# Kernel optimization log

Measured on AMD Instinct MI355X. Metric: run time of the kernel, lower is better.

The kernel has to match this reference:

```python
import jax, jax.numpy as jnp
import numpy as np

HIDDEN = 1024
SINK = 4
RECENT = 19  # int(window_size=64 * 0.3)
COMPRESSION_RATIO = 0.5


def setup_inputs() -> dict:
    key = jax.random.key(0)
    ks = jax.random.split(key, 10)
    B, S, H = 4, 4096, HIDDEN
    xav = lambda k, fi, fo: jax.random.normal(k, (fi, fo), jnp.float32) * np.sqrt(2.0 / (fi + fo))
    return {
        'keys': jax.random.normal(ks[0], (B, S, H), jnp.float32),
        'values': jax.random.normal(ks[1], (B, S, H), jnp.float32),
        # attention_predictor: Linear(H, H//2) -> ReLU -> Linear(H//2, 1) -> Sigmoid
        'W1a': xav(ks[2], H, H // 2), 'b1a': jnp.zeros((H // 2,), jnp.float32),
        'W2a': xav(ks[3], H // 2, 1), 'b2a': jnp.zeros((1,), jnp.float32),
        # importance_estimator: Linear(H, H//4) -> ReLU -> Linear(H//4, 1)
        'W1i': xav(ks[4], H, H // 4), 'b1i': jnp.zeros((H // 4,), jnp.float32),
        'W2i': xav(ks[5], H // 4, 1), 'b2i': jnp.zeros((1,), jnp.float32),
    }


def _token_scores(keys, values, W1a, b1a, W2a, b2a, W1i, b1i, W2i, b2i):
    att = jax.nn.sigmoid(jnp.einsum('bsh,ho->bso', jax.nn.relu(keys @ W1a + b1a), W2a) + b2a)[..., 0]
    imp = (jnp.einsum('bsh,ho->bso', jax.nn.relu(values @ W1i + b1i), W2i) + b2i)[..., 0]
    return 0.6 * att + 0.4 * imp  # [B, S]


def _selection_mask(scores):
    B, S = scores.shape
    keep_count = max(int(S * (1.0 - COMPRESSION_RATIO)), SINK + RECENT)
    mask = jnp.zeros((B, S), dtype=bool)
    mask = mask.at[:, :SINK].set(True)
    mask = mask.at[:, S - RECENT:].set(True)
    mid_len = S - RECENT - SINK
    if mid_len > 0:
        middle_keep = keep_count - SINK - RECENT
        if middle_keep > 0:
            k = min(middle_keep, mid_len)
            _, idx = jax.lax.top_k(scores[:, SINK:S - RECENT], k)  # [B, k]
            rows = jnp.arange(B)[:, None]
            mask = mask.at[rows, idx + SINK].set(True)
    return mask


def reference(keys, values, W1a, b1a, W2a, b2a, W1i, b1i, W2i, b2i):
    scores = _token_scores(keys, values, W1a, b1a, W2a, b2a, W1i, b1i, W2i, b2i)
    mask = _selection_mask(scores).astype(keys.dtype)[..., None]  # [B, S, 1]
    return keys * mask, values * mask
```

## Files before the change

kernel.cpp:

```cpp
#include <hip/hip_runtime.h>
#include <math.h>

#define H      1024
#define NA     512
#define NI     256
#define SEQ    4096
#define BATCH  4
#define NTOK   (BATCH*SEQ)
#define MTOK   16
#define KC     8
#define PT     20
#define SINKN  4
#define RECENTN 19
#define MIDN   (SEQ - SINKN - RECENTN)
#define KSEL   2025
#define CHK    16

__global__ __launch_bounds__(256, 4) void score_kernel(
    const float* __restrict__ keys, const float* __restrict__ values,
    const float* __restrict__ W1a, const float* __restrict__ b1a,
    const float* __restrict__ W2a, const float* __restrict__ b2a,
    const float* __restrict__ W1i, const float* __restrict__ b1i,
    const float* __restrict__ W2i, const float* __restrict__ b2i,
    float* __restrict__ scores)
{
    __shared__ __align__(16) float smem[KC * NA + KC * NI + 2 * KC * PT];
    float* wa_lds = smem;
    float* wi_lds = smem + KC * NA;
    float* k_lds  = smem + KC * (NA + NI);
    float* v_lds  = k_lds + KC * PT;

    const int tid  = threadIdx.x;
    const int to   = tid & 63;
    const int tt   = tid >> 6;
    const int tokb = blockIdx.x * MTOK;

    float accA0[4][4], accA1[4][4], accI[4][4];
#pragma unroll
    for (int j = 0; j < 4; ++j)
#pragma unroll
        for (int t = 0; t < 4; ++t) { accA0[j][t] = 0.f; accA1[j][t] = 0.f; accI[j][t] = 0.f; }

    const bool st_on = (tid & 3) == 0;
    const int  item  = tid >> 2;
    const int  st_t  = item & 15;
    const int  st_q  = (item >> 4) & 1;
    const bool st_v  = (item >> 5) & 1;
    const float* st_src = (st_v ? values : keys) + (size_t)(tokb + st_t) * H + st_q * 4;
    float* st_dst = (st_v ? v_lds : k_lds);

    for (int h0 = 0; h0 < H; h0 += KC) {
        const float4* wap = (const float4*)(W1a + (size_t)h0 * NA);
        const float4* wip = (const float4*)(W1i + (size_t)h0 * NI);
        float4 wb0 = wap[tid];
        float4 wb1 = wap[tid + 256];
        float4 wb2 = wap[tid + 512];
        float4 wb3 = wap[tid + 768];
        float4 ib0 = wip[tid];
        float4 ib1 = wip[tid + 256];
        float4 tk;
        if (st_on) tk = *(const float4*)(st_src + h0);

        __syncthreads();
        ((float4*)wa_lds)[tid      ] = wb0;
        ((float4*)wa_lds)[tid + 256] = wb1;
        ((float4*)wa_lds)[tid + 512] = wb2;
        ((float4*)wa_lds)[tid + 768] = wb3;
        ((float4*)wi_lds)[tid      ] = ib0;
        ((float4*)wi_lds)[tid + 256] = ib1;
        if (st_on) {
            st_dst[(st_q * 4 + 0) * PT + st_t] = tk.x;
            st_dst[(st_q * 4 + 1) * PT + st_t] = tk.y;
            st_dst[(st_q * 4 + 2) * PT + st_t] = tk.z;
            st_dst[(st_q * 4 + 3) * PT + st_t] = tk.w;
        }
        __syncthreads();

#pragma unroll
        for (int h = 0; h < KC; ++h) {
            float kf[4], vf[4], wa[8], wi4[4];
            *(float4*)&kf[0]  = *(const float4*)&k_lds[h * PT + tt * 4];
            *(float4*)&vf[0]  = *(const float4*)&v_lds[h * PT + tt * 4];
            *(float4*)&wa[0]  = *(const float4*)&wa_lds[h * NA + to * 4];
            *(float4*)&wa[4]  = *(const float4*)&wa_lds[h * NA + 256 + to * 4];
            *(float4*)&wi4[0] = *(const float4*)&wi_lds[h * NI + to * 4];
#pragma unroll
            for (int j = 0; j < 4; ++j)
#pragma unroll
                for (int t = 0; t < 4; ++t) {
                    accA0[j][t] = fmaf(kf[t], wa[j],     accA0[j][t]);
                    accA1[j][t] = fmaf(kf[t], wa[4 + j], accA1[j][t]);
                    accI[j][t]  = fmaf(vf[t], wi4[j],    accI[j][t]);
                }
        }
    }

    float b1aA[8], w2aA[8], b1iA[4], w2iA[4];
    *(float4*)&b1aA[0] = *(const float4*)(b1a + to * 4);
    *(float4*)&b1aA[4] = *(const float4*)(b1a + 256 + to * 4);
    *(float4*)&w2aA[0] = *(const float4*)(W2a + to * 4);
    *(float4*)&w2aA[4] = *(const float4*)(W2a + 256 + to * 4);
    *(float4*)&b1iA[0] = *(const float4*)(b1i + to * 4);
    *(float4*)&w2iA[0] = *(const float4*)(W2i + to * 4);

    __syncthreads();
    float* red_a = smem;
    float* red_i = smem + 16 * 65;

#pragma unroll
    for (int t = 0; t < 4; ++t) {
        float pa = 0.f, pi = 0.f;
#pragma unroll
        for (int j = 0; j < 4; ++j) {
            pa += fmaxf(accA0[j][t] + b1aA[j],     0.f) * w2aA[j];
            pa += fmaxf(accA1[j][t] + b1aA[4 + j], 0.f) * w2aA[4 + j];
            pi += fmaxf(accI[j][t]  + b1iA[j],     0.f) * w2iA[j];
        }
        const int tg = tt * 4 + t;
        red_a[tg * 65 + to] = pa;
        red_i[tg * 65 + to] = pi;
    }
    __syncthreads();
    if (tid < MTOK) {
        float sa = 0.f, si = 0.f;
        for (int j2 = 0; j2 < 64; ++j2) {
            sa += red_a[tid * 65 + j2];
            si += red_i[tid * 65 + j2];
        }
        const float att = 1.f / (1.f + expf(-(sa + b2a[0])));
        scores[tokb + tid] = 0.6f * att + 0.4f * (si + b2i[0]);
    }
}

__device__ __forceinline__ int block_sum(int val, int* red, int tid)
{
#pragma unroll
    for (int off = 32; off > 0; off >>= 1) val += __shfl_down(val, off);
    if ((tid & 63) == 0) red[tid >> 6] = val;
    __syncthreads();
    const int total = red[0] + red[1] + red[2] + red[3];
    __syncthreads();
    return total;
}

__global__ __launch_bounds__(256) void select_kernel(
    const float* __restrict__ scores, float* __restrict__ mask)
{
    __shared__ unsigned int ks[MIDN];
    __shared__ int hist[256];
    __shared__ int red[4];
    __shared__ int scan_s[256];
    __shared__ unsigned int sh_pref;
    __shared__ int sh_r;

    const int tid = threadIdx.x;
    const int row = blockIdx.x;
    const float* sr = scores + row * SEQ;

    for (int i = tid; i < MIDN; i += 256) {
        unsigned int u = __float_as_uint(sr[SINKN + i]);
        u = (u & 0x80000000u) ? ~u : (u | 0x80000000u);
        ks[i] = u;
    }
    if (tid == 0) { sh_pref = 0u; sh_r = KSEL; }
    __syncthreads();

    for (int b = 3; b >= 0; --b) {
        hist[tid] = 0;
        __syncthreads();
        const unsigned int hi_mask = (b == 3) ? 0u : (0xFFFFFFFFu << ((b + 1) * 8));
        const unsigned int pref = sh_pref;
        for (int i = tid; i < MIDN; i += 256) {
            const unsigned int u = ks[i];
            if ((u & hi_mask) == pref)
                atomicAdd(&hist[(u >> (b * 8)) & 255], 1);
        }
        __syncthreads();

        scan_s[tid] = hist[tid];
        __syncthreads();
#pragma unroll
        for (int off = 1; off < 256; off <<= 1) {
            const int add = (tid + off < 256) ? scan_s[tid + off] : 0;
            __syncthreads();
            scan_s[tid] += add;
            __syncthreads();
        }
        const int r    = sh_r;
        const int sfx  = scan_s[tid];
        const int sfx1 = (tid < 255) ? scan_s[tid + 1] : 0;
        if (sfx >= r && sfx1 < r) {
            sh_r = r - sfx1;
            sh_pref = pref | ((unsigned int)tid << (b * 8));
        }
        __syncthreads();
    }
    const unsigned int v = sh_pref;

    const int st = tid * CHK;
    const int en = (st + CHK < MIDN) ? (st + CHK) : MIDN;

    int cgt = 0, ceq = 0;
    for (int k = st; k < en; ++k) { cgt += (ks[k] > v) ? 1 : 0; ceq += (ks[k] == v) ? 1 : 0; }
    const int total_gt = block_sum(cgt, red, tid);
    const int need = KSEL - total_gt;

    scan_s[tid] = ceq;
    __syncthreads();
#pragma unroll
    for (int off = 1; off < 256; off <<= 1) {
        const int add = (tid >= off) ? scan_s[tid - off] : 0;
        __syncthreads();
        scan_s[tid] += add;
        __syncthreads();
    }
    int r = scan_s[tid] - ceq;

    float* mr = mask + row * SEQ;
    for (int k = st; k < en; ++k) {
        const unsigned int u = ks[k];
        bool keep = false;
        if (u > v) keep = true;
        else if (u == v) { keep = (r < need); ++r; }
        mr[SINKN + k] = keep ? 1.f : 0.f;
    }
    for (int s = tid; s < SEQ; s += 256) {
        if (s < SINKN || s >= SEQ - RECENTN) mr[s] = 1.f;
    }
}

__global__ __launch_bounds__(256) void apply_kernel(
    const float* __restrict__ keys, const float* __restrict__ values,
    const float* __restrict__ mask, float* __restrict__ out)
{
    const int QT = NTOK * H / 4;
    const int stride = gridDim.x * 256;
    for (int i4 = blockIdx.x * 256 + threadIdx.x; i4 < 2 * QT; i4 += stride) {
        const bool isv = (i4 >= QT);
        const int  j4  = isv ? (i4 - QT) : i4;
        const float m  = mask[j4 >> 8];
        const float4* src = isv ? (const float4*)values : (const float4*)keys;
        const float4 x = src[j4];
        float4 y; y.x = x.x * m; y.y = x.y * m; y.z = x.z * m; y.w = x.w * m;
        ((float4*)out)[i4] = y;
    }
}

extern "C" void kernel_launch(void* const* d_in, const int* in_sizes, int n_in,
                              void* d_out, int out_size, void* d_ws, size_t ws_size,
                              hipStream_t stream)
{
    const float* keys   = (const float*)d_in[0];
    const float* values = (const float*)d_in[1];
    const float* W1a = (const float*)d_in[2];
    const float* b1a = (const float*)d_in[3];
    const float* W2a = (const float*)d_in[4];
    const float* b2a = (const float*)d_in[5];
    const float* W1i = (const float*)d_in[6];
    const float* b1i = (const float*)d_in[7];
    const float* W2i = (const float*)d_in[8];
    const float* b2i = (const float*)d_in[9];

    float* scores = (float*)d_ws;
    float* mask   = scores + NTOK;

    score_kernel<<<NTOK / MTOK, 256, 0, stream>>>(keys, values, W1a, b1a, W2a, b2a,
                                                  W1i, b1i, W2i, b2i, scores);
    select_kernel<<<BATCH, 256, 0, stream>>>(scores, mask);
    apply_kernel<<<8192, 256, 0, stream>>>(keys, values, mask, (float*)d_out);
}
```

Baseline: 635.6 us.

## Retile score MLP as 128x128 register-blocked GEMM with per-slice partial outputs

```diff
diff --git a/kernel.cpp b/kernel.cpp
--- a/kernel.cpp
+++ b/kernel.cpp
@@ -7,128 +7,126 @@
 #define SEQ    4096
 #define BATCH  4
 #define NTOK   (BATCH*SEQ)
-#define MTOK   16
-#define KC     8
-#define PT     20
 #define SINKN  4
 #define RECENTN 19
 #define MIDN   (SEQ - SINKN - RECENTN)
 #define KSEL   2025
 #define CHK    16
 
-__global__ __launch_bounds__(256, 4) void score_kernel(
+#define TT   128
+#define UT   128
+#define KC   32
+#define PTA  132
+#define ATT_BLOCKS ((NTOK/TT) * (NA/UT))
+#define IMP_BLOCKS ((NTOK/TT) * (NI/UT))
+
+__global__ __launch_bounds__(256, 3) void score_gemm_kernel(
     const float* __restrict__ keys, const float* __restrict__ values,
     const float* __restrict__ W1a, const float* __restrict__ b1a,
-    const float* __restrict__ W2a, const float* __restrict__ b2a,
+    const float* __restrict__ W2a,
     const float* __restrict__ W1i, const float* __restrict__ b1i,
-    const float* __restrict__ W2i, const float* __restrict__ b2i,
-    float* __restrict__ scores)
-{
-    __shared__ __align__(16) float smem[KC * NA + KC * NI + 2 * KC * PT];
-    float* wa_lds = smem;
-    float* wi_lds = smem + KC * NA;
-    float* k_lds  = smem + KC * (NA + NI);
-    float* v_lds  = k_lds + KC * PT;
-
-    const int tid  = threadIdx.x;
-    const int to   = tid & 63;
-    const int tt   = tid >> 6;
-    const int tokb = blockIdx.x * MTOK;
-
-    float accA0[4][4], accA1[4][4], accI[4][4];
-#pragma unroll
-    for (int j = 0; j < 4; ++j)
-#pragma unroll
-        for (int t = 0; t < 4; ++t) { accA0[j][t] = 0.f; accA1[j][t] = 0.f; accI[j][t] = 0.f; }
-
-    const bool st_on = (tid & 3) == 0;
-    const int  item  = tid >> 2;
-    const int  st_t  = item & 15;
-    const int  st_q  = (item >> 4) & 1;
-    const bool st_v  = (item >> 5) & 1;
-    const float* st_src = (st_v ? values : keys) + (size_t)(tokb + st_t) * H + st_q * 4;
-    float* st_dst = (st_v ? v_lds : k_lds);
+    const float* __restrict__ W2i,
+    float* __restrict__ part)
+{
+    __shared__ __align__(16) float smem[KC * PTA + KC * UT];
+    float* A_lds = smem;
+    float* B_lds = smem + KC * PTA;
+
+    const int tid = threadIdx.x;
+    const int tx  = tid & 15;
+    const int ty  = tid >> 4;
+    const int bid = blockIdx.x;
+
+    const bool is_att = bid < ATT_BLOCKS;
+    const int  lb     = is_att ? bid : bid - ATT_BLOCKS;
+    const int  tile   = is_att ? (lb >> 2) : (lb >> 1);
+    const int  pass   = is_att ? (lb & 3)  : (lb & 1);
+    const int  slot   = is_att ? pass : 4 + pass;
+    const int  tokb   = tile * TT;
+    const int  u0     = pass * UT;
+    const int  wstride = is_att ? NA : NI;
+
+    const float* Aptr = is_att ? keys : values;
+    const float* Wptr = (is_att ? W1a : W1i) + u0;
+    const float* b1p  = (is_att ? b1a : b1i) + u0;
+    const float* w2p  = (is_att ? W2a : W2i) + u0;
+
+    float acc[8][8];
+#pragma unroll
+    for (int t = 0; t < 8; ++t)
+#pragma unroll
+        for (int u = 0; u < 8; ++u) acc[t][u] = 0.f;
+
+    const int at = tid >> 3;
+    const int aq = tid & 7;
+    const float* a_base = Aptr + (size_t)(tokb + at) * H + aq * 4;
+    const int bu = (tid & 31) * 4;
+    const int rb = tid >> 5;
+    const float* b_base = Wptr + (size_t)rb * wstride + bu;
+    const int bq   = bu >> 2;
+    const int bpos = ((bq ^ (bq >> 3)) << 2);
+    const int q1 = 2 * tx, q2 = 2 * tx + 1;
+    const int boff1 = ((q1 ^ (q1 >> 3)) << 2);
+    const int boff2 = ((q2 ^ (q2 >> 3)) << 2);
 
     for (int h0 = 0; h0 < H; h0 += KC) {
-        const float4* wap = (const float4*)(W1a + (size_t)h0 * NA);
-        const float4* wip = (const float4*)(W1i + (size_t)h0 * NI);
-        float4 wb0 = wap[tid];
-        float4 wb1 = wap[tid + 256];
-        float4 wb2 = wap[tid + 512];
-        float4 wb3 = wap[tid + 768];
-        float4 ib0 = wip[tid];
-        float4 ib1 = wip[tid + 256];
-        float4 tk;
-        if (st_on) tk = *(const float4*)(st_src + h0);
-
-        __syncthreads();
-        ((float4*)wa_lds)[tid      ] = wb0;
-        ((float4*)wa_lds)[tid + 256] = wb1;
-        ((float4*)wa_lds)[tid + 512] = wb2;
-        ((float4*)wa_lds)[tid + 768] = wb3;
-        ((float4*)wi_lds)[tid      ] = ib0;
-        ((float4*)wi_lds)[tid + 256] = ib1;
-        if (st_on) {
-            st_dst[(st_q * 4 + 0) * PT + st_t] = tk.x;
-            st_dst[(st_q * 4 + 1) * PT + st_t] = tk.y;
-            st_dst[(st_q * 4 + 2) * PT + st_t] = tk.z;
-            st_dst[(st_q * 4 + 3) * PT + st_t] = tk.w;
-        }
-        __syncthreads();
-
-#pragma unroll
+        float4 aR[4], bR[4];
+#pragma unroll
+        for (int p = 0; p < 4; ++p)
+            aR[p] = *(const float4*)(a_base + h0 + (size_t)p * 32 * H);
+#pragma unroll
+        for (int p = 0; p < 4; ++p)
+            bR[p] = *(const float4*)(b_base + (size_t)(h0 + p * 8) * wstride);
+
+        __syncthreads();
+#pragma unroll
+        for (int p = 0; p < 4; ++p) {
+            A_lds[(aq * 4 + 0) * PTA + at + p * 32] = aR[p].x;
+            A_lds[(aq * 4 + 1) * PTA + at + p * 32] = aR[p].y;
+            A_lds[(aq * 4 + 2) * PTA + at + p * 32] = aR[p].z;
+            A_lds[(aq * 4 + 3) * PTA + at + p * 32] = aR[p].w;
+        }
+#pragma unroll
+        for (int p = 0; p < 4; ++p)
+            *(float4*)&B_lds[(rb + p * 8) * UT + bpos] = bR[p];
+        __syncthreads();
+
+#pragma unroll 8
         for (int h = 0; h < KC; ++h) {
-            float kf[4], vf[4], wa[8], wi4[4];
-            *(float4*)&kf[0]  = *(const float4*)&k_lds[h * PT + tt * 4];
-            *(float4*)&vf[0]  = *(const float4*)&v_lds[h * PT + tt * 4];
-            *(float4*)&wa[0]  = *(const float4*)&wa_lds[h * NA + to * 4];
-            *(float4*)&wa[4]  = *(const float4*)&wa_lds[h * NA + 256 + to * 4];
-            *(float4*)&wi4[0] = *(const float4*)&wi_lds[h * NI + to * 4];
-#pragma unroll
-            for (int j = 0; j < 4; ++j)
-#pragma unroll
-                for (int t = 0; t < 4; ++t) {
-                    accA0[j][t] = fmaf(kf[t], wa[j],     accA0[j][t]);
-                    accA1[j][t] = fmaf(kf[t], wa[4 + j], accA1[j][t]);
-                    accI[j][t]  = fmaf(vf[t], wi4[j],    accI[j][t]);
-                }
-        }
-    }
-
-    float b1aA[8], w2aA[8], b1iA[4], w2iA[4];
-    *(float4*)&b1aA[0] = *(const float4*)(b1a + to * 4);
-    *(float4*)&b1aA[4] = *(const float4*)(b1a + 256 + to * 4);
-    *(float4*)&w2aA[0] = *(const float4*)(W2a + to * 4);
-    *(float4*)&w2aA[4] = *(const float4*)(W2a + 256 + to * 4);
-    *(float4*)&b1iA[0] = *(const float4*)(b1i + to * 4);
-    *(float4*)&w2iA[0] = *(const float4*)(W2i + to * 4);
-
-    __syncthreads();
-    float* red_a = smem;
-    float* red_i = smem + 16 * 65;
-
-#pragma unroll
-    for (int t = 0; t < 4; ++t) {
-        float pa = 0.f, pi = 0.f;
-#pragma unroll
-        for (int j = 0; j < 4; ++j) {
-            pa += fmaxf(accA0[j][t] + b1aA[j],     0.f) * w2aA[j];
-            pa += fmaxf(accA1[j][t] + b1aA[4 + j], 0.f) * w2aA[4 + j];
-            pi += fmaxf(accI[j][t]  + b1iA[j],     0.f) * w2iA[j];
-        }
-        const int tg = tt * 4 + t;
-        red_a[tg * 65 + to] = pa;
-        red_i[tg * 65 + to] = pi;
-    }
-    __syncthreads();
-    if (tid < MTOK) {
-        float sa = 0.f, si = 0.f;
-        for (int j2 = 0; j2 < 64; ++j2) {
-            sa += red_a[tid * 65 + j2];
-            si += red_i[tid * 65 + j2];
-        }
-        const float att = 1.f / (1.f + expf(-(sa + b2a[0])));
-        scores[tokb + tid] = 0.6f * att + 0.4f * (si + b2i[0]);
+            float a[8], b[8];
+            *(float4*)&a[0] = *(const float4*)&A_lds[h * PTA + ty * 8];
+            *(float4*)&a[4] = *(const float4*)&A_lds[h * PTA + ty * 8 + 4];
+            *(float4*)&b[0] = *(const float4*)&B_lds[h * UT + boff1];
+            *(float4*)&b[4] = *(const float4*)&B_lds[h * UT + boff2];
+#pragma unroll
+            for (int t = 0; t < 8; ++t)
+#pragma unroll
+                for (int u = 0; u < 8; ++u)
+                    acc[t][u] = fmaf(a[t], b[u], acc[t][u]);
+        }
+    }
+
+    float b1v[8], w2v[8];
+    *(float4*)&b1v[0] = *(const float4*)(b1p + tx * 8);
+    *(float4*)&b1v[4] = *(const float4*)(b1p + tx * 8 + 4);
+    *(float4*)&w2v[0] = *(const float4*)(w2p + tx * 8);
+    *(float4*)&w2v[4] = *(const float4*)(w2p + tx * 8 + 4);
+
+    __syncthreads();
+    float* red = smem;
+#pragma unroll
+    for (int t = 0; t < 8; ++t) {
+        float s = 0.f;
+#pragma unroll
+        for (int u = 0; u < 8; ++u)
+            s += fmaxf(acc[t][u] + b1v[u], 0.f) * w2v[u];
+        red[(ty * 8 + t) * 17 + tx] = s;
+    }
+    __syncthreads();
+    if (tid < TT) {
+        float s = 0.f;
+        for (int x = 0; x < 16; ++x) s += red[tid * 17 + x];
+        part[(size_t)slot * NTOK + tokb + tid] = s;
     }
 }
 
@@ -144,7 +142,8 @@
 }
 
 __global__ __launch_bounds__(256) void select_kernel(
-    const float* __restrict__ scores, float* __restrict__ mask)
+    const float* __restrict__ part, const float* __restrict__ b2a,
+    const float* __restrict__ b2i, float* __restrict__ mask)
 {
     __shared__ unsigned int ks[MIDN];
     __shared__ int hist[256];
@@ -155,10 +154,16 @@
 
     const int tid = threadIdx.x;
     const int row = blockIdx.x;
-    const float* sr = scores + row * SEQ;
+    const float ba  = b2a[0];
+    const float bi2 = b2i[0];
 
     for (int i = tid; i < MIDN; i += 256) {
-        unsigned int u = __float_as_uint(sr[SINKN + i]);
+        const int tok = row * SEQ + SINKN + i;
+        float sa = ((part[tok] + part[NTOK + tok]) + part[2 * NTOK + tok]) + part[3 * NTOK + tok];
+        float si = part[4 * NTOK + tok] + part[5 * NTOK + tok];
+        const float att = 1.f / (1.f + expf(-(sa + ba)));
+        const float s = 0.6f * att + 0.4f * (si + bi2);
+        unsigned int u = __float_as_uint(s);
         u = (u & 0x80000000u) ? ~u : (u | 0x80000000u);
         ks[i] = u;
     }
@@ -261,11 +266,11 @@
     const float* W2i = (const float*)d_in[8];
     const float* b2i = (const float*)d_in[9];
 
-    float* scores = (float*)d_ws;
-    float* mask   = scores + NTOK;
-
-    score_kernel<<<NTOK / MTOK, 256, 0, stream>>>(keys, values, W1a, b1a, W2a, b2a,
-                                                  W1i, b1i, W2i, b2i, scores);
-    select_kernel<<<BATCH, 256, 0, stream>>>(scores, mask);
+    float* part = (float*)d_ws;
+    float* mask = part + 6 * NTOK;
+
+    score_gemm_kernel<<<ATT_BLOCKS + IMP_BLOCKS, 256, 0, stream>>>(
+        keys, values, W1a, b1a, W2a, W1i, b1i, W2i, part);
+    select_kernel<<<BATCH, 256, 0, stream>>>(part, b2a, b2i, mask);
     apply_kernel<<<8192, 256, 0, stream>>>(keys, values, mask, (float*)d_out);
 }
```

Measured after the change: 560.8 us. 11.8% less time.
